# Performance work log

Measured on AMD Instinct MI355X. Metric: run time of the kernel, lower is better.

The kernel has to match this reference:

```python
import jax, jax.numpy as jnp
import numpy as np


def _pool_masks(corners, size):
    # Reproduce torch: corners/4; LL=clamp(LL,0,21); UR=clamp(where(UR-LL>=2,UR,LL+2),2,23);
    # then int() truncation (== floor for nonneg) of both bounds before slicing.
    c = corners / 4.0
    LL = jnp.clip(c[:, :, 0, :], 0.0, 21.0)            # [B,P,3]
    UR = c[:, :, 1, :]
    UR = jnp.clip(jnp.where(UR - LL >= 2.0, UR, LL + 2.0), 2.0, 23.0)
    lo = jnp.floor(LL).astype(jnp.int32)               # [B,P,3]
    n = jnp.floor(UR).astype(jnp.int32) - lo           # crop length per axis, >= 2
    # AdaptiveMaxPool3d(output_size=2) bins: bin k covers [floor(k*n/2), ceil((k+1)*n/2))
    k = jnp.arange(2)
    bin_lo = lo[:, :, None, :] + (k[None, None, :, None] * n[:, :, None, :]) // 2            # [B,P,2,3]
    bin_hi = lo[:, :, None, :] + ((k[None, None, :, None] + 1) * n[:, :, None, :] + 1) // 2  # [B,P,2,3]
    idx = jnp.arange(size)
    # per-axis boolean membership masks, each [B,P,2,size]
    return [(idx >= bin_lo[:, :, :, a, None]) & (idx < bin_hi[:, :, :, a, None]) for a in range(3)]


def reference(fm, corners):
    # fm: [B,C,D,H,W] with D=H=W=24; corners: [B,P,2,3] float voxel coords
    B, C, D, H, W = fm.shape
    mx, my, mz = _pool_masks(corners, D)
    neg = jnp.asarray(-jnp.inf, fm.dtype)
    # Adaptive max-pool over a separable box == nested per-axis masked maxes (fused by XLA under jit).
    # axis x: [B,P,C,2,H,W]
    t = jnp.where(mx[:, :, None, :, :, None, None], fm[:, None, :, None, :, :, :], neg).max(axis=4)
    # axis y: [B,P,C,2,2,W]
    t = jnp.where(my[:, :, None, None, :, :, None], t[:, :, :, :, None, :, :], neg).max(axis=5)
    # axis z: [B,P,C,2,2,2]
    t = jnp.where(mz[:, :, None, None, None, :, :], t[:, :, :, :, :, None, :], neg).max(axis=6)
    return t


def setup_inputs() -> dict:
    key = jax.random.key(0)
    k1, k2 = jax.random.split(key)
    fm = jax.random.normal(k1, (4, 64, 24, 24, 24), dtype=jnp.float32)
    # raw corner coords in original-volume voxels [0, 96); module divides by 4 internally
    corners = jax.random.uniform(k2, (4, 64, 2, 3), dtype=jnp.float32) * 96.0
    return {"fm": fm, "corners": corners}
```

## Files before the change

kernel.cpp:

```cpp
#include <hip/hip_runtime.h>
#include <math.h>


#define FM_CH 13824

__global__ __launch_bounds__(256) void crop_pool_kernel(
    const float* __restrict__ fm,
    const float* __restrict__ corners,
    float* __restrict__ out)
{
    const int lane = threadIdx.x & 63;
    const int w    = blockIdx.x * 4 + (threadIdx.x >> 6);
    const int n = w & 63;
    const int c = (w >> 6) & 63;
    const int b = w >> 12;
    const int bn = b * 64 + n;

    const int bin = lane >> 3;
    const int sub = lane & 7;
    const int ks[3] = { (bin >> 2) & 1, (bin >> 1) & 1, bin & 1 };

    int s0[3], s1[3];
#pragma unroll
    for (int a = 0; a < 3; ++a) {
        float LL = corners[bn * 6 + a] * 0.25f;
        LL = fminf(fmaxf(LL, 0.0f), 21.0f);
        float UR = corners[bn * 6 + 3 + a] * 0.25f;
        UR = (UR - LL >= 2.0f) ? UR : (LL + 2.0f);
        UR = fminf(fmaxf(UR, 2.0f), 23.0f);
        int lo = (int)floorf(LL);
        int nn = (int)floorf(UR) - lo;
        s0[a] = lo + ((ks[a] * nn) >> 1);
        s1[a] = lo + (((ks[a] + 1) * nn + 1) >> 1);
    }
    const unsigned ny  = (unsigned)(s1[1] - s0[1]);
    const unsigned nz  = (unsigned)(s1[2] - s0[2]);
    const unsigned vol = (unsigned)(s1[0] - s0[0]) * ny * nz;

    const unsigned Mz = (1u << 19) / nz + 1;
    const unsigned My = (1u << 19) / ny + 1;

    const float* base = fm + (size_t)(b * 64 + c) * FM_CH
                           + ((s0[0] * 24 + s0[1]) * 24 + s0[2]);

    auto voxel = [&](unsigned i) -> float {
        unsigned q = (i * Mz) >> 19;
        unsigned z = i - q * nz;
        unsigned x = (q * My) >> 19;
        unsigned y = q - x * ny;
        return base[x * 576u + y * 24u + z];
    };

    float m0 = -INFINITY, m1 = -INFINITY, m2 = -INFINITY, m3 = -INFINITY;
    unsigned i = sub;
    for (; i + 24 < vol; i += 32) {
        m0 = fmaxf(m0, voxel(i));
        m1 = fmaxf(m1, voxel(i + 8));
        m2 = fmaxf(m2, voxel(i + 16));
        m3 = fmaxf(m3, voxel(i + 24));
    }
    for (; i < vol; i += 8)
        m0 = fmaxf(m0, voxel(i));
    float m = fmaxf(fmaxf(m0, m1), fmaxf(m2, m3));

#pragma unroll
    for (int off = 1; off < 8; off <<= 1)
        m = fmaxf(m, __shfl_xor(m, off));

    float v = __shfl(m, (lane & 7) << 3);
    if (lane < 8)
        out[((size_t)(bn * 64 + c)) * 8 + lane] = v;
}

extern "C" void kernel_launch(void* const* d_in, const int* in_sizes, int n_in,
                              void* d_out, int out_size, void* d_ws, size_t ws_size,
                              hipStream_t stream)
{
    const float* fm      = (const float*)d_in[0];
    const float* corners = (const float*)d_in[1];
    float* out           = (float*)d_out;

    crop_pool_kernel<<<4096, 256, 0, stream>>>(fm, corners, out);
}
```

Baseline: 69.94 us.

## Stage each channel volume in shared memory and reuse it across all boxes

Each block now loads one full (b,c) 24^3 feature volume into LDS with float4 copies, then its 8 waves loop over the 64 boxes, gathering voxels from LDS instead of global memory. Before, each wave gathered scattered voxels from global or L2 for every box. The grid shrinks from 4096 to 256 blocks of 512 threads, and each block uses 54KB of LDS, which limits occupancy. Each wave also processes 8 boxes serially, so the work is more exposed to imbalance in box sizes.

```diff
diff --git a/kernel.cpp b/kernel.cpp
--- a/kernel.cpp
+++ b/kernel.cpp
@@ -2,74 +2,88 @@
 #include <math.h>
 
 
-#define FM_CH 13824
+#define SPAT 13824
 
-__global__ __launch_bounds__(256) void crop_pool_kernel(
+__global__ __launch_bounds__(512) void crop_pool_kernel(
     const float* __restrict__ fm,
     const float* __restrict__ corners,
     float* __restrict__ out)
 {
-    const int lane = threadIdx.x & 63;
-    const int w    = blockIdx.x * 4 + (threadIdx.x >> 6);
-    const int n = w & 63;
-    const int c = (w >> 6) & 63;
-    const int b = w >> 12;
-    const int bn = b * 64 + n;
+    __shared__ float sv[SPAT];
+    const int blk = blockIdx.x;
+    const int b   = blk >> 6;
+    const int c   = blk & 63;
+    const int t   = threadIdx.x;
 
-    const int bin = lane >> 3;
-    const int sub = lane & 7;
+    {
+        const float4* src = (const float4*)(fm + (size_t)blk * SPAT);
+        float4* dst = (float4*)sv;
+#pragma unroll
+        for (int p = 0; p < 7; ++p) {
+            const int i = p * 512 + t;
+            if (i < SPAT / 4) dst[i] = src[i];
+        }
+    }
+    __syncthreads();
+
+    const int wid  = t >> 6;
+    const int lane = t & 63;
+    const int bin  = lane >> 3;
+    const int sub  = lane & 7;
     const int ks[3] = { (bin >> 2) & 1, (bin >> 1) & 1, bin & 1 };
 
-    int s0[3], s1[3];
+    for (int p = 0; p < 8; ++p) {
+        const int n  = wid * 8 + p;
+        const int bn = b * 64 + n;
+
+        int s0[3], s1[3];
 #pragma unroll
-    for (int a = 0; a < 3; ++a) {
-        float LL = corners[bn * 6 + a] * 0.25f;
-        LL = fminf(fmaxf(LL, 0.0f), 21.0f);
-        float UR = corners[bn * 6 + 3 + a] * 0.25f;
-        UR = (UR - LL >= 2.0f) ? UR : (LL + 2.0f);
-        UR = fminf(fmaxf(UR, 2.0f), 23.0f);
-        int lo = (int)floorf(LL);
-        int nn = (int)floorf(UR) - lo;
-        s0[a] = lo + ((ks[a] * nn) >> 1);
-        s1[a] = lo + (((ks[a] + 1) * nn + 1) >> 1);
-    }
-    const unsigned ny  = (unsigned)(s1[1] - s0[1]);
-    const unsigned nz  = (unsigned)(s1[2] - s0[2]);
-    const unsigned vol = (unsigned)(s1[0] - s0[0]) * ny * nz;
+        for (int a = 0; a < 3; ++a) {
+            float LL = corners[bn * 6 + a] * 0.25f;
+            LL = fminf(fmaxf(LL, 0.0f), 21.0f);
+            float UR = corners[bn * 6 + 3 + a] * 0.25f;
+            UR = (UR - LL >= 2.0f) ? UR : (LL + 2.0f);
+            UR = fminf(fmaxf(UR, 2.0f), 23.0f);
+            const int lo = (int)floorf(LL);
+            const int nn = (int)floorf(UR) - lo;
+            s0[a] = lo + ((ks[a] * nn) >> 1);
+            s1[a] = lo + (((ks[a] + 1) * nn + 1) >> 1);
+        }
+        const unsigned ny   = (unsigned)(s1[1] - s0[1]);
+        const unsigned nz   = (unsigned)(s1[2] - s0[2]);
+        const unsigned nvox = (unsigned)(s1[0] - s0[0]) * ny * nz;
+        const unsigned Mz = (1u << 19) / nz + 1;
+        const unsigned My = (1u << 19) / ny + 1;
+        const int boff = (s0[0] * 24 + s0[1]) * 24 + s0[2];
 
-    const unsigned Mz = (1u << 19) / nz + 1;
-    const unsigned My = (1u << 19) / ny + 1;
+        auto voxel = [&](unsigned i) -> float {
+            unsigned q = (i * Mz) >> 19;
+            unsigned z = i - q * nz;
+            unsigned x = (q * My) >> 19;
+            unsigned y = q - x * ny;
+            return sv[boff + (int)(x * 576u + y * 24u + z)];
+        };
 
-    const float* base = fm + (size_t)(b * 64 + c) * FM_CH
-                           + ((s0[0] * 24 + s0[1]) * 24 + s0[2]);
-
-    auto voxel = [&](unsigned i) -> float {
-        unsigned q = (i * Mz) >> 19;
-        unsigned z = i - q * nz;
-        unsigned x = (q * My) >> 19;
-        unsigned y = q - x * ny;
-        return base[x * 576u + y * 24u + z];
-    };
-
-    float m0 = -INFINITY, m1 = -INFINITY, m2 = -INFINITY, m3 = -INFINITY;
-    unsigned i = sub;
-    for (; i + 24 < vol; i += 32) {
-        m0 = fmaxf(m0, voxel(i));
-        m1 = fmaxf(m1, voxel(i + 8));
-        m2 = fmaxf(m2, voxel(i + 16));
-        m3 = fmaxf(m3, voxel(i + 24));
-    }
-    for (; i < vol; i += 8)
-        m0 = fmaxf(m0, voxel(i));
-    float m = fmaxf(fmaxf(m0, m1), fmaxf(m2, m3));
+        float m0 = -INFINITY, m1 = -INFINITY, m2 = -INFINITY, m3 = -INFINITY;
+        unsigned i = sub;
+        for (; i + 24 < nvox; i += 32) {
+            m0 = fmaxf(m0, voxel(i));
+            m1 = fmaxf(m1, voxel(i + 8));
+            m2 = fmaxf(m2, voxel(i + 16));
+            m3 = fmaxf(m3, voxel(i + 24));
+        }
+        for (; i < nvox; i += 8)
+            m0 = fmaxf(m0, voxel(i));
+        float m = fmaxf(fmaxf(m0, m1), fmaxf(m2, m3));
 
 #pragma unroll
-    for (int off = 1; off < 8; off <<= 1)
-        m = fmaxf(m, __shfl_xor(m, off));
+        for (int off = 1; off < 8; off <<= 1)
+            m = fmaxf(m, __shfl_xor(m, off));
 
-    float v = __shfl(m, (lane & 7) << 3);
-    if (lane < 8)
-        out[((size_t)(bn * 64 + c)) * 8 + lane] = v;
+        const float v = __shfl(m, (lane & 7) << 3);
+        if (lane < 8)
+            out[((size_t)(bn * 64 + c)) * 8 + lane] = v;
+    }
 }
 
 extern "C" void kernel_launch(void* const* d_in, const int* in_sizes, int n_in,
@@ -80,5 +94,5 @@
     const float* corners = (const float*)d_in[1];
     float* out           = (float*)d_out;
 
-    crop_pool_kernel<<<4096, 256, 0, stream>>>(fm, corners, out);
+    crop_pool_kernel<<<256, 512, 0, stream>>>(fm, corners, out);
 }
```

Result: no change. 69.38 us (-0.8%).
